# Performance work log

Hardware: AMD Instinct MI355X
Metric: run time of the kernel (lower is better)

Reference implementation:

```python
import jax, jax.numpy as jnp
import numpy as np

B, T, D, H = 4, 1024, 1024, 16
DH = D // H  # 64

def setup_inputs() -> dict:
    key = jax.random.key(0)
    ks = jax.random.split(key, 5)
    s = 1.0 / np.sqrt(D)
    return {
        "x": jax.random.normal(ks[0], (B, T, D), dtype=jnp.float32),
        "Wqkv": jax.random.uniform(ks[1], (D, 3 * D), dtype=jnp.float32, minval=-s, maxval=s),
        "bqkv": jax.random.uniform(ks[2], (3 * D,), dtype=jnp.float32, minval=-s, maxval=s),
        "Wproj": jax.random.uniform(ks[3], (D, D), dtype=jnp.float32, minval=-s, maxval=s),
        "bproj": jax.random.uniform(ks[4], (D,), dtype=jnp.float32, minval=-s, maxval=s),
        "mask": jnp.ones((B, T), dtype=jnp.int32),
    }

def reference(x, Wqkv, bqkv, Wproj, bproj, mask):
    Bx, Tx, C = x.shape
    qkv = x @ Wqkv + bqkv                      # [B,T,3D]
    q, k, v = jnp.split(qkv, 3, axis=-1)
    # [B,H,T,DH]
    q = q.reshape(Bx, Tx, H, DH).transpose(0, 2, 1, 3)
    k = k.reshape(Bx, Tx, H, DH).transpose(0, 2, 1, 3)
    v = v.reshape(Bx, Tx, H, DH).transpose(0, 2, 1, 3)
    att = jnp.einsum("bhqd,bhkd->bhqk", q, k) / np.sqrt(DH)
    causal = jnp.tril(jnp.ones((Tx, Tx), dtype=bool))          # [T,T]
    keep = causal[None, None] & (mask[:, None, None, :] != 0)  # [B,1,T,T] broadcast
    att = jnp.where(keep, att, -jnp.inf)
    att = jax.nn.softmax(att, axis=-1)
    # dropout is identity in eval / p=0
    out = jnp.einsum("bhqk,bhkd->bhqd", att, v)                # [B,H,T,DH]
    out = out.transpose(0, 2, 1, 3).reshape(Bx, Tx, C)
    return out @ Wproj + bproj
```

## Files before the change

kernel.cpp:

```cpp
#include <hip/hip_runtime.h>
#include <hip/hip_bf16.h>
#include <cstddef>
#include <cstdint>

#define Bb 4
#define Tt 1024
#define Dd 1024
#define Hh 16

typedef __bf16 bf16x8 __attribute__((ext_vector_type(8)));
typedef __bf16 bf16x4 __attribute__((ext_vector_type(4)));
typedef float  f32x4  __attribute__((ext_vector_type(4)));

__device__ __forceinline__ void gload16(const void* g, void* l) {
    __builtin_amdgcn_global_load_lds(
        (const __attribute__((address_space(1))) void*)g,
        (__attribute__((address_space(3))) void*)l, 16, 0, 0);
}

__global__ __launch_bounds__(256) void cast_f32_bf16(const float* __restrict__ in,
                                                     __bf16* __restrict__ out, int n4) {
    int i = blockIdx.x * 256 + threadIdx.x;
    if (i < n4) {
        float4 v = ((const float4*)in)[i];
        bf16x4 o = { (__bf16)v.x, (__bf16)v.y, (__bf16)v.z, (__bf16)v.w };
        ((bf16x4*)out)[i] = o;
    }
}

__global__ __launch_bounds__(256) void transpose_cast(const float* __restrict__ in,
                                                      __bf16* __restrict__ out,
                                                      int K, int N) {
    __shared__ float ld[64][65];
    const int k0 = blockIdx.x * 64;
    const int n0 = blockIdx.y * 64;
    #pragma unroll
    for (int i = 0; i < 16; i++) {
        int idx = i * 256 + threadIdx.x;
        int r = idx >> 6, c = idx & 63;
        ld[r][c] = in[(size_t)(k0 + r) * N + n0 + c];
    }
    __syncthreads();
    #pragma unroll
    for (int i = 0; i < 16; i++) {
        int idx = i * 256 + threadIdx.x;
        int r = idx >> 6, c = idx & 63;
        out[(size_t)(n0 + r) * K + k0 + c] = (__bf16)ld[c][r];
    }
}

__global__ __launch_bounds__(256) void v_transpose(const __bf16* __restrict__ qkv,
                                                   __bf16* __restrict__ vt) {
    __shared__ __bf16 ld[64][65];
    const int t0 = blockIdx.x * 64;
    const int h  = blockIdx.y;
    const int b  = blockIdx.z;
    const size_t src = ((size_t)(b * Tt + t0)) * 3072 + 2048 + h * 64;
    #pragma unroll
    for (int i = 0; i < 16; i++) {
        int idx = i * 256 + threadIdx.x;
        int tr = idx >> 6, dc = idx & 63;
        ld[tr][dc] = qkv[src + (size_t)tr * 3072 + dc];
    }
    __syncthreads();
    const size_t dst = ((size_t)((b * Hh + h) * 64)) * Tt + t0;
    #pragma unroll
    for (int i = 0; i < 16; i++) {
        int idx = i * 256 + threadIdx.x;
        int dr = idx >> 6, tc = idx & 63;
        vt[dst + (size_t)dr * Tt + tc] = ld[tc][dr];
    }
}

__global__ __launch_bounds__(256) void gemm_bf16(const __bf16* __restrict__ A,
                                                 const __bf16* __restrict__ Bt,
                                                 const float* __restrict__ bias,
                                                 void* __restrict__ Cout,
                                                 int M, int N, int K, int mode) {
    __shared__ __align__(16) __bf16 As[128 * 64];
    __shared__ __align__(16) __bf16 Bs[128 * 64];
    const int tid  = threadIdx.x;
    const int lane = tid & 63;
    const int wave = tid >> 6;
    const int wy = wave >> 1, wx = wave & 1;
    const int l15 = lane & 15, quad = lane >> 4;
    const size_t row0 = (size_t)blockIdx.y * 128;
    const size_t col0 = (size_t)blockIdx.x * 128;

    f32x4 acc[4][4] = {};

    for (int k0 = 0; k0 < K; k0 += 64) {
        #pragma unroll
        for (int i = 0; i < 4; i++) {
            int c = i * 256 + tid;
            int r = c >> 3, seg = (c & 7) ^ (r & 7);
            gload16(&A[(row0 + r) * K + k0 + seg * 8], &As[c * 8]);
        }
        #pragma unroll
        for (int i = 0; i < 4; i++) {
            int c = i * 256 + tid;
            int r = c >> 3, seg = (c & 7) ^ (r & 7);
            gload16(&Bt[(col0 + r) * K + k0 + seg * 8], &Bs[c * 8]);
        }
        __syncthreads();
        #pragma unroll
        for (int kc = 0; kc < 2; kc++) {
            bf16x8 af[4], bfr[4];
            #pragma unroll
            for (int i = 0; i < 4; i++)
                af[i] = *(const bf16x8*)&As[(wy * 64 + i * 16 + l15) * 64 +
                                            (((kc * 4 + quad) ^ (l15 & 7)) * 8)];
            #pragma unroll
            for (int j = 0; j < 4; j++)
                bfr[j] = *(const bf16x8*)&Bs[(wx * 64 + j * 16 + l15) * 64 +
                                             (((kc * 4 + quad) ^ (l15 & 7)) * 8)];
            #pragma unroll
            for (int i = 0; i < 4; i++)
                #pragma unroll
                for (int j = 0; j < 4; j++)
                    acc[i][j] = __builtin_amdgcn_mfma_f32_16x16x32_bf16(af[i], bfr[j], acc[i][j], 0, 0, 0);
        }
        __syncthreads();
    }

    #pragma unroll
    for (int j = 0; j < 4; j++) {
        const size_t col = col0 + wx * 64 + j * 16 + l15;
        const float bj = bias[col];
        const float scale = (mode == 1 && col < 1024) ? 0.125f : 1.0f;
        #pragma unroll
        for (int i = 0; i < 4; i++) {
            const size_t row = row0 + wy * 64 + i * 16 + quad * 4;
            #pragma unroll
            for (int r = 0; r < 4; r++) {
                float v = (acc[i][j][r] + bj) * scale;
                if (mode == 1) ((__bf16*)Cout)[(row + r) * N + col] = (__bf16)v;
                else           ((float*)Cout)[(row + r) * N + col] = v;
            }
        }
    }
}

__global__ __launch_bounds__(256) void gemm_bf16_n64(const __bf16* __restrict__ A,
                                                     const __bf16* __restrict__ Bt,
                                                     const float* __restrict__ bias,
                                                     float* __restrict__ Cout,
                                                     int M, int N, int K) {
    __shared__ __align__(16) __bf16 As[128 * 64];
    __shared__ __align__(16) __bf16 Bs[64 * 64];
    const int tid  = threadIdx.x;
    const int lane = tid & 63;
    const int wave = tid >> 6;
    const int wy = wave >> 1, wx = wave & 1;
    const int l15 = lane & 15, quad = lane >> 4;
    const size_t row0 = (size_t)blockIdx.y * 128;
    const size_t col0 = (size_t)blockIdx.x * 64;

    f32x4 acc[4][2] = {};

    for (int k0 = 0; k0 < K; k0 += 64) {
        #pragma unroll
        for (int i = 0; i < 4; i++) {
            int c = i * 256 + tid;
            int r = c >> 3, seg = (c & 7) ^ (r & 7);
            gload16(&A[(row0 + r) * K + k0 + seg * 8], &As[c * 8]);
        }
        #pragma unroll
        for (int i = 0; i < 2; i++) {
            int c = i * 256 + tid;
            int r = c >> 3, seg = (c & 7) ^ (r & 7);
            gload16(&Bt[(col0 + r) * K + k0 + seg * 8], &Bs[c * 8]);
        }
        __syncthreads();
        #pragma unroll
        for (int kc = 0; kc < 2; kc++) {
            bf16x8 af[4], bfr[2];
            #pragma unroll
            for (int i = 0; i < 4; i++)
                af[i] = *(const bf16x8*)&As[(wy * 64 + i * 16 + l15) * 64 +
                                            (((kc * 4 + quad) ^ (l15 & 7)) * 8)];
            #pragma unroll
            for (int j = 0; j < 2; j++)
                bfr[j] = *(const bf16x8*)&Bs[(wx * 32 + j * 16 + l15) * 64 +
                                             (((kc * 4 + quad) ^ (l15 & 7)) * 8)];
            #pragma unroll
            for (int i = 0; i < 4; i++)
                #pragma unroll
                for (int j = 0; j < 2; j++)
                    acc[i][j] = __builtin_amdgcn_mfma_f32_16x16x32_bf16(af[i], bfr[j], acc[i][j], 0, 0, 0);
        }
        __syncthreads();
    }

    #pragma unroll
    for (int j = 0; j < 2; j++) {
        const size_t col = col0 + wx * 32 + j * 16 + l15;
        const float bj = bias[col];
        #pragma unroll
        for (int i = 0; i < 4; i++) {
            const size_t row = row0 + wy * 64 + i * 16 + quad * 4;
            #pragma unroll
            for (int r = 0; r < 4; r++)
                Cout[(row + r) * N + col] = acc[i][j][r] + bj;
        }
    }
}

__global__ __launch_bounds__(256, 2) void attn_mfma(const __bf16* __restrict__ qkv,
                                                    const __bf16* __restrict__ vt,
                                                    const int* __restrict__ mask,
                                                    __bf16* __restrict__ att) {
    __shared__ __align__(16) __bf16 Qs[128 * 64];
    __shared__ __align__(16) __bf16 Ks[2][64 * 64];
    __shared__ __align__(16) __bf16 Vs[2][64 * 64];
    __shared__ __align__(16) __bf16 Ps[4][16 * 64];

    const int p = blockIdx.x, h = blockIdx.y, b = blockIdx.z;
    const int qlo = p, qhi = 15 - p, nk = 16 - p;
    const int tid = threadIdx.x, lane = tid & 63, wave = tid >> 6;
    const int l15 = lane & 15, quad = lane >> 4;

    #pragma unroll
    for (int i = 0; i < 4; i++) {
        int c = i * 256 + tid;
        int rr = c >> 3, ch = c & 7;
        int w_ = rr >> 5, s_ = (rr >> 4) & 1, r16 = rr & 15;
        int grow = (s_ ? qhi : qlo) * 64 + w_ * 16 + r16;
        gload16(&qkv[((size_t)(b * Tt + grow)) * 3072 + h * 64 + ((ch ^ (rr & 7)) * 8)],
                &Qs[c * 8]);
    }
    #pragma unroll
    for (int i = 0; i < 2; i++) {
        int c = i * 256 + tid;
        int rr = c >> 3, ch = c & 7, sw = ((ch ^ (rr & 7)) * 8);
        gload16(&qkv[((size_t)(b * Tt + rr)) * 3072 + 1024 + h * 64 + sw], &Ks[0][c * 8]);
        gload16(&vt[((size_t)((b * Hh + h) * 64 + rr)) * Tt + sw], &Vs[0][c * 8]);
    }

    f32x4 Oacc[2][4] = {};
    float lsum[2] = { 0.0f, 0.0f };

    for (int kt = 0; kt < nk; kt++) {
        __syncthreads();
        const int cur = kt & 1;
        if (kt + 1 < nk) {
            #pragma unroll
            for (int i = 0; i < 2; i++) {
                int c = i * 256 + tid;
                int rr = c >> 3, ch = c & 7, sw = ((ch ^ (rr & 7)) * 8);
                gload16(&qkv[((size_t)(b * Tt + (kt + 1) * 64 + rr)) * 3072 + 1024 + h * 64 + sw],
                        &Ks[cur ^ 1][c * 8]);
                gload16(&vt[((size_t)((b * Hh + h) * 64 + rr)) * Tt + (kt + 1) * 64 + sw],
                        &Vs[cur ^ 1][c * 8]);
            }
        }

        int mv4[4][4];
        #pragma unroll
        for (int j = 0; j < 4; j++) {
            const int4 m4 = *(const int4*)&mask[b * Tt + kt * 64 + j * 16 + quad * 4];
            mv4[j][0] = m4.x; mv4[j][1] = m4.y; mv4[j][2] = m4.z; mv4[j][3] = m4.w;
        }

        bf16x8 ak[4][2], av[4][2];
        #pragma unroll
        for (int j = 0; j < 4; j++)
            #pragma unroll
            for (int kc = 0; kc < 2; kc++) {
                int sw = (((kc * 4 + quad) ^ (l15 & 7)) * 8);
                ak[j][kc] = *(const bf16x8*)&Ks[cur][(j * 16 + l15) * 64 + sw];
                av[j][kc] = *(const bf16x8*)&Vs[cur][(j * 16 + l15) * 64 + sw];
            }

        #pragma unroll
        for (int s = 1; s >= 0; s--) {
            if (s == 0 && kt > qlo) continue;
            const int tile = s ? qhi : qlo;
            const int rowbase = wave * 32 + s * 16;
            bf16x8 q0 = *(const bf16x8*)&Qs[(rowbase + l15) * 64 + ((quad ^ (l15 & 7)) * 8)];
            bf16x8 q1 = *(const bf16x8*)&Qs[(rowbase + l15) * 64 + (((4 + quad) ^ (l15 & 7)) * 8)];

            #pragma unroll
            for (int j = 0; j < 4; j++) {
                f32x4 st = {};
                st = __builtin_amdgcn_mfma_f32_16x16x32_bf16(ak[j][0], q0, st, 0, 0, 0);
                st = __builtin_amdgcn_mfma_f32_16x16x32_bf16(ak[j][1], q1, st, 0, 0, 0);
                bf16x4 pv;
                #pragma unroll
                for (int r = 0; r < 4; r++) {
                    const int tloc = j * 16 + quad * 4 + r;
                    bool keep = (mv4[j][r] != 0);
                    if (kt == tile) keep = keep && (tloc <= wave * 16 + l15);
                    const float pe = keep ? __expf(st[r]) : 0.0f;
                    lsum[s] += pe;
                    pv[r] = (__bf16)pe;
                }
                *(bf16x4*)&Ps[wave][l15 * 64 + (((j * 4 + quad) ^ ((l15 & 7) << 1)) * 4)] = pv;
            }
            bf16x8 p0 = *(const bf16x8*)&Ps[wave][l15 * 64 + (((2 * quad) ^ ((l15 & 7) << 1)) * 4)];
            bf16x8 p1 = *(const bf16x8*)&Ps[wave][l15 * 64 + (((2 * (4 + quad)) ^ ((l15 & 7) << 1)) * 4)];
            #pragma unroll
            for (int n = 0; n < 4; n++) {
                Oacc[s][n] = __builtin_amdgcn_mfma_f32_16x16x32_bf16(av[n][0], p0, Oacc[s][n], 0, 0, 0);
                Oacc[s][n] = __builtin_amdgcn_mfma_f32_16x16x32_bf16(av[n][1], p1, Oacc[s][n], 0, 0, 0);
            }
        }
    }

    #pragma unroll
    for (int s = 0; s < 2; s++) {
        const int tile = s ? qhi : qlo;
        float lt = lsum[s];
        lt += __shfl_xor(lt, 16);
        lt += __shfl_xor(lt, 32);
        const float inv = 1.0f / lt;
        const int q = tile * 64 + wave * 16 + l15;
        #pragma unroll
        for (int n = 0; n < 4; n++) {
            bf16x4 o;
            #pragma unroll
            for (int r = 0; r < 4; r++) o[r] = (__bf16)(Oacc[s][n][r] * inv);
            *(bf16x4*)&att[((size_t)(b * Tt + q)) * Dd + h * 64 + n * 16 + quad * 4] = o;
        }
    }
}

extern "C" void kernel_launch(void* const* d_in, const int* in_sizes, int n_in,
                              void* d_out, int out_size, void* d_ws, size_t ws_size,
                              hipStream_t stream) {
    const float* x     = (const float*)d_in[0];
    const float* Wqkv  = (const float*)d_in[1];
    const float* bqkv  = (const float*)d_in[2];
    const float* Wproj = (const float*)d_in[3];
    const float* bproj = (const float*)d_in[4];
    const int*   mask  = (const int*)d_in[5];
    float* out = (float*)d_out;

    __bf16* xb  = (__bf16*)d_ws;
    __bf16* wqT = xb  + (size_t)4096 * 1024;
    __bf16* wpT = wqT + (size_t)3072 * 1024;
    __bf16* qkv = wpT + (size_t)1024 * 1024;
    __bf16* vt  = qkv + (size_t)4096 * 3072;
    __bf16* att = vt  + (size_t)4 * 16 * 64 * 1024;

    cast_f32_bf16<<<4096, 256, 0, stream>>>(x, xb, (4096 * 1024) / 4);
    transpose_cast<<<dim3(16, 48), 256, 0, stream>>>(Wqkv, wqT, 1024, 3072);
    transpose_cast<<<dim3(16, 16), 256, 0, stream>>>(Wproj, wpT, 1024, 1024);

    gemm_bf16<<<dim3(24, 32), 256, 0, stream>>>(xb, wqT, bqkv, qkv, 4096, 3072, 1024, 1);

    v_transpose<<<dim3(16, 16, 4), 256, 0, stream>>>(qkv, vt);
    attn_mfma<<<dim3(8, 16, 4), 256, 0, stream>>>(qkv, vt, mask, att);

    gemm_bf16_n64<<<dim3(16, 32), 256, 0, stream>>>(att, wpT, bproj, out, 4096, 1024, 1024);
}
```

Before: 176.2 us.

## Fuse prep kernels and single-buffer attention LDS to fit three blocks per CU

The three preprocessing kernels (x cast and the two weight transpose-casts) are merged into one launch with block-index dispatch, which removes two kernel launches. The attention kernel drops Q from LDS by loading its fragments into registers once, and replaces K/V double buffering with a single buffer plus an extra barrier. This shrinks LDS from about 40KB to 24KB so launch bounds can request three blocks per CU. The cost is that the next tile's loads can no longer overlap compute on the current tile, there is an additional sync per iteration, and register pressure is tighter.

```diff
diff --git a/kernel.cpp b/kernel.cpp
--- a/kernel.cpp
+++ b/kernel.cpp
@@ -18,22 +18,33 @@
         (__attribute__((address_space(3))) void*)l, 16, 0, 0);
 }
 
-__global__ __launch_bounds__(256) void cast_f32_bf16(const float* __restrict__ in,
-                                                     __bf16* __restrict__ out, int n4) {
-    int i = blockIdx.x * 256 + threadIdx.x;
-    if (i < n4) {
-        float4 v = ((const float4*)in)[i];
+__global__ __launch_bounds__(256) void prep(const float* __restrict__ x,
+                                            const float* __restrict__ Wqkv,
+                                            const float* __restrict__ Wproj,
+                                            __bf16* __restrict__ xb,
+                                            __bf16* __restrict__ wqT,
+                                            __bf16* __restrict__ wpT) {
+    const int bid = blockIdx.x;
+    if (bid < 4096) {
+        int i = bid * 256 + threadIdx.x;
+        float4 v = ((const float4*)x)[i];
         bf16x4 o = { (__bf16)v.x, (__bf16)v.y, (__bf16)v.z, (__bf16)v.w };
-        ((bf16x4*)out)[i] = o;
-    }
-}
-
-__global__ __launch_bounds__(256) void transpose_cast(const float* __restrict__ in,
-                                                      __bf16* __restrict__ out,
-                                                      int K, int N) {
+        ((bf16x4*)xb)[i] = o;
+        return;
+    }
     __shared__ float ld[64][65];
-    const int k0 = blockIdx.x * 64;
-    const int n0 = blockIdx.y * 64;
+    const float* in;
+    __bf16* out;
+    int K, N, k0, n0;
+    if (bid < 4096 + 768) {
+        int j = bid - 4096;
+        in = Wqkv; out = wqT; K = 1024; N = 3072;
+        k0 = (j & 15) * 64; n0 = (j >> 4) * 64;
+    } else {
+        int j = bid - 4096 - 768;
+        in = Wproj; out = wpT; K = 1024; N = 1024;
+        k0 = (j & 15) * 64; n0 = (j >> 4) * 64;
+    }
     #pragma unroll
     for (int i = 0; i < 16; i++) {
         int idx = i * 256 + threadIdx.x;
@@ -206,14 +217,14 @@
     }
 }
 
-__global__ __launch_bounds__(256, 2) void attn_mfma(const __bf16* __restrict__ qkv,
+__global__ __launch_bounds__(256, 3) void attn_mfma(const __bf16* __restrict__ qkv,
                                                     const __bf16* __restrict__ vt,
                                                     const int* __restrict__ mask,
                                                     __bf16* __restrict__ att) {
-    __shared__ __align__(16) __bf16 Qs[128 * 64];
-    __shared__ __align__(16) __bf16 Ks[2][64 * 64];
-    __shared__ __align__(16) __bf16 Vs[2][64 * 64];
-    __shared__ __align__(16) __bf16 Ps[4][16 * 64];
+    __shared__ __align__(16) __bf16 smem[3 * 64 * 64];
+    __bf16* const Ks = smem;
+    __bf16* const Vs = smem + 4096;
+    __bf16* const Ps = smem + 8192;
 
     const int p = blockIdx.x, h = blockIdx.y, b = blockIdx.z;
     const int qlo = p, qhi = 15 - p, nk = 16 - p;
@@ -227,14 +238,24 @@
         int w_ = rr >> 5, s_ = (rr >> 4) & 1, r16 = rr & 15;
         int grow = (s_ ? qhi : qlo) * 64 + w_ * 16 + r16;
         gload16(&qkv[((size_t)(b * Tt + grow)) * 3072 + h * 64 + ((ch ^ (rr & 7)) * 8)],
-                &Qs[c * 8]);
-    }
+                &smem[c * 8]);
+    }
+    __syncthreads();
+    bf16x8 qf[2][2];
+    #pragma unroll
+    for (int s = 0; s < 2; s++) {
+        const int rowb = wave * 32 + s * 16 + l15;
+        qf[s][0] = *(const bf16x8*)&smem[rowb * 64 + ((quad ^ (l15 & 7)) * 8)];
+        qf[s][1] = *(const bf16x8*)&smem[rowb * 64 + (((4 + quad) ^ (l15 & 7)) * 8)];
+    }
+    __syncthreads();
+
     #pragma unroll
     for (int i = 0; i < 2; i++) {
         int c = i * 256 + tid;
         int rr = c >> 3, ch = c & 7, sw = ((ch ^ (rr & 7)) * 8);
-        gload16(&qkv[((size_t)(b * Tt + rr)) * 3072 + 1024 + h * 64 + sw], &Ks[0][c * 8]);
-        gload16(&vt[((size_t)((b * Hh + h) * 64 + rr)) * Tt + sw], &Vs[0][c * 8]);
+        gload16(&qkv[((size_t)(b * Tt + rr)) * 3072 + 1024 + h * 64 + sw], &Ks[c * 8]);
+        gload16(&vt[((size_t)((b * Hh + h) * 64 + rr)) * Tt + sw], &Vs[c * 8]);
     }
 
     f32x4 Oacc[2][4] = {};
@@ -242,16 +263,27 @@
 
     for (int kt = 0; kt < nk; kt++) {
         __syncthreads();
-        const int cur = kt & 1;
+
+        bf16x8 ak[4][2], av[4][2];
+        #pragma unroll
+        for (int j = 0; j < 4; j++)
+            #pragma unroll
+            for (int kc = 0; kc < 2; kc++) {
+                int sw = (((kc * 4 + quad) ^ (l15 & 7)) * 8);
+                ak[j][kc] = *(const bf16x8*)&Ks[(j * 16 + l15) * 64 + sw];
+                av[j][kc] = *(const bf16x8*)&Vs[(j * 16 + l15) * 64 + sw];
+            }
+        __syncthreads();
+
         if (kt + 1 < nk) {
             #pragma unroll
             for (int i = 0; i < 2; i++) {
                 int c = i * 256 + tid;
                 int rr = c >> 3, ch = c & 7, sw = ((ch ^ (rr & 7)) * 8);
                 gload16(&qkv[((size_t)(b * Tt + (kt + 1) * 64 + rr)) * 3072 + 1024 + h * 64 + sw],
-                        &Ks[cur ^ 1][c * 8]);
+                        &Ks[c * 8]);
                 gload16(&vt[((size_t)((b * Hh + h) * 64 + rr)) * Tt + (kt + 1) * 64 + sw],
-                        &Vs[cur ^ 1][c * 8]);
+                        &Vs[c * 8]);
             }
         }
 
@@ -262,29 +294,15 @@
             mv4[j][0] = m4.x; mv4[j][1] = m4.y; mv4[j][2] = m4.z; mv4[j][3] = m4.w;
         }
 
-        bf16x8 ak[4][2], av[4][2];
-        #pragma unroll
-        for (int j = 0; j < 4; j++)
-            #pragma unroll
-            for (int kc = 0; kc < 2; kc++) {
-                int sw = (((kc * 4 + quad) ^ (l15 & 7)) * 8);
-                ak[j][kc] = *(const bf16x8*)&Ks[cur][(j * 16 + l15) * 64 + sw];
-                av[j][kc] = *(const bf16x8*)&Vs[cur][(j * 16 + l15) * 64 + sw];
-            }
-
         #pragma unroll
         for (int s = 1; s >= 0; s--) {
             if (s == 0 && kt > qlo) continue;
             const int tile = s ? qhi : qlo;
-            const int rowbase = wave * 32 + s * 16;
-            bf16x8 q0 = *(const bf16x8*)&Qs[(rowbase + l15) * 64 + ((quad ^ (l15 & 7)) * 8)];
-            bf16x8 q1 = *(const bf16x8*)&Qs[(rowbase + l15) * 64 + (((4 + quad) ^ (l15 & 7)) * 8)];
-
             #pragma unroll
             for (int j = 0; j < 4; j++) {
                 f32x4 st = {};
-                st = __builtin_amdgcn_mfma_f32_16x16x32_bf16(ak[j][0], q0, st, 0, 0, 0);
-                st = __builtin_amdgcn_mfma_f32_16x16x32_bf16(ak[j][1], q1, st, 0, 0, 0);
+                st = __builtin_amdgcn_mfma_f32_16x16x32_bf16(ak[j][0], qf[s][0], st, 0, 0, 0);
+                st = __builtin_amdgcn_mfma_f32_16x16x32_bf16(ak[j][1], qf[s][1], st, 0, 0, 0);
                 bf16x4 pv;
                 #pragma unroll
                 for (int r = 0; r < 4; r++) {
@@ -295,10 +313,10 @@
                     lsum[s] += pe;
                     pv[r] = (__bf16)pe;
                 }
-                *(bf16x4*)&Ps[wave][l15 * 64 + (((j * 4 + quad) ^ ((l15 & 7) << 1)) * 4)] = pv;
-            }
-            bf16x8 p0 = *(const bf16x8*)&Ps[wave][l15 * 64 + (((2 * quad) ^ ((l15 & 7) << 1)) * 4)];
-            bf16x8 p1 = *(const bf16x8*)&Ps[wave][l15 * 64 + (((2 * (4 + quad)) ^ ((l15 & 7) << 1)) * 4)];
+                *(bf16x4*)&Ps[wave * 1024 + l15 * 64 + (((j * 4 + quad) ^ ((l15 & 7) << 1)) * 4)] = pv;
+            }
+            bf16x8 p0 = *(const bf16x8*)&Ps[wave * 1024 + l15 * 64 + (((2 * quad) ^ ((l15 & 7) << 1)) * 4)];
+            bf16x8 p1 = *(const bf16x8*)&Ps[wave * 1024 + l15 * 64 + (((2 * (4 + quad)) ^ ((l15 & 7) << 1)) * 4)];
             #pragma unroll
             for (int n = 0; n < 4; n++) {
                 Oacc[s][n] = __builtin_amdgcn_mfma_f32_16x16x32_bf16(av[n][0], p0, Oacc[s][n], 0, 0, 0);
@@ -343,9 +361,7 @@
     __bf16* vt  = qkv + (size_t)4096 * 3072;
     __bf16* att = vt  + (size_t)4 * 16 * 64 * 1024;
 
-    cast_f32_bf16<<<4096, 256, 0, stream>>>(x, xb, (4096 * 1024) / 4);
-    transpose_cast<<<dim3(16, 48), 256, 0, stream>>>(Wqkv, wqT, 1024, 3072);
-    transpose_cast<<<dim3(16, 16), 256, 0, stream>>>(Wproj, wpT, 1024, 1024);
+    prep<<<4096 + 768 + 256, 256, 0, stream>>>(x, Wqkv, Wproj, xb, wqT, wpT);
 
     gemm_bf16<<<dim3(24, 32), 256, 0, stream>>>(xb, wqT, bqkv, qkv, 4096, 3072, 1024, 1);
 
```

After: 194.1 us. +10.2%, slower.
